# Performance work log

Measured on AMD Instinct MI355X. Metric: run time of the kernel, lower is better.

## Reference

```python
import jax, jax.numpy as jnp
import numpy as np

NEG_SLOPE = 0.2  # PyG GATConv default negative_slope
EPS = 1e-16      # PyG softmax denominator eps


def gat_layer(x, src, dst, W, b, a_src, a_dst, n_nodes):
    # x: [N, Fin]; W: [Fout, Fin]; a_src/a_dst: [Fout] (heads=1, concat)
    h = x @ W.T                                   # [N, Fout]
    al_s = h @ a_src                              # [N]
    al_d = h @ a_dst                              # [N]
    e = jax.nn.leaky_relu(al_s[src] + al_d[dst], NEG_SLOPE)   # [E]
    m = jax.lax.stop_gradient(
        jax.ops.segment_max(e, dst, num_segments=n_nodes))   # stable softmax per target
    ex = jnp.exp(e - m[dst])
    denom = jax.ops.segment_sum(ex, dst, num_segments=n_nodes)
    alpha = ex / (denom[dst] + EPS)               # [E]
    out = jax.ops.segment_sum(alpha[:, None] * h[src], dst, num_segments=n_nodes)
    return out + b


def reference(x, edge_index, W0, b0, asrc0, adst0, W1, b1, asrc1, adst1):
    B, N, _ = x.shape
    # GATConv adds self-loops by default
    loops = jnp.arange(N, dtype=edge_index.dtype)
    src = jnp.concatenate([edge_index[0], loops])
    dst = jnp.concatenate([edge_index[1], loops])

    def per_graph(xb):
        h = jax.nn.relu(gat_layer(xb, src, dst, W0, b0, asrc0, adst0, N))
        h = jax.nn.relu(gat_layer(h, src, dst, W1, b1, asrc1, adst1, N))
        return h

    return jax.vmap(per_graph)(x)  # [B, N, Fout]


def setup_inputs() -> dict:
    key = jax.random.key(0)
    ks = jax.random.split(key, 10)
    B, N, E = 4, 10000, 320000
    F0, F1, F2 = 256, 256, 128
    x = jax.random.normal(ks[0], (B, N, F0), dtype=jnp.float32)
    edge_index = jax.random.randint(ks[1], (2, E), 0, N, dtype=jnp.int64)
    s0 = 1.0 / np.sqrt(F0)
    s1 = 1.0 / np.sqrt(F1)
    return {
        "x": x,
        "edge_index": edge_index,
        "W0": jax.random.normal(ks[2], (F1, F0), dtype=jnp.float32) * s0,
        "b0": jnp.zeros((F1,), dtype=jnp.float32),
        "asrc0": jax.random.normal(ks[3], (F1,), dtype=jnp.float32) * s1,
        "adst0": jax.random.normal(ks[4], (F1,), dtype=jnp.float32) * s1,
        "W1": jax.random.normal(ks[5], (F2, F1), dtype=jnp.float32) * s1,
        "b1": jnp.zeros((F2,), dtype=jnp.float32),
        "asrc1": jax.random.normal(ks[6], (F2,), dtype=jnp.float32) / np.sqrt(F2),
        "adst1": jax.random.normal(ks[7], (F2,), dtype=jnp.float32) / np.sqrt(F2),
    }
```

## Files before the change

### kernel.cpp

```cpp
#include <hip/hip_runtime.h>
#include <hip/hip_bf16.h>

#define NN 10000
#define EE 320000
#define BB 4
#define F0 256
#define F1 256
#define F2 128
#define ETOT (EE + NN)

typedef __attribute__((ext_vector_type(8))) short bf16x8;
typedef __attribute__((ext_vector_type(4))) float f32x4;

__device__ inline unsigned short f2bf_rn(float f) {
    unsigned int u = __float_as_uint(f);
    unsigned int r = (u + 0x7fffu + ((u >> 16) & 1u)) >> 16;
    return (unsigned short)r;
}
__device__ inline float bf2f(unsigned short s) {
    return __uint_as_float(((unsigned int)s) << 16);
}

__global__ void count_kernel(const int* __restrict__ ei, int* __restrict__ deg) {
    int id = blockIdx.x * blockDim.x + threadIdx.x;
    if (id >= ETOT) return;
    int dst = (id < EE) ? ei[EE + id] : (id - EE);
    atomicAdd(&deg[dst], 1);
}

__global__ void scan_kernel(const int* __restrict__ deg, int* __restrict__ rowstart) {
    __shared__ int part[256];
    int t = threadIdx.x;
    const int CH = (NN + 255) / 256;
    int lo = t * CH, hi = min(lo + CH, NN);
    int s = 0;
    for (int i = lo; i < hi; i++) s += deg[i];
    part[t] = s;
    __syncthreads();
    for (int off = 1; off < 256; off <<= 1) {
        int v = (t >= off) ? part[t - off] : 0;
        __syncthreads();
        part[t] += v;
        __syncthreads();
    }
    int run = (t == 0) ? 0 : part[t - 1];
    for (int i = lo; i < hi; i++) { int d = deg[i]; rowstart[i] = run; run += d; }
    if (t == 255) rowstart[NN] = run;
}

__global__ void scatter_kernel(const int* __restrict__ ei,
                               const int* __restrict__ rowstart,
                               int* __restrict__ fill,
                               int* __restrict__ sorted_src) {
    int id = blockIdx.x * blockDim.x + threadIdx.x;
    if (id >= ETOT) return;
    int src, dst;
    if (id < EE) { src = ei[id]; dst = ei[EE + id]; }
    else         { src = dst = id - EE; }
    int pos = rowstart[dst] + atomicAdd(&fill[dst], 1);
    sorted_src[pos] = src;
}

__global__ __launch_bounds__(256) void conv_split(const float* __restrict__ in,
                                                  unsigned short* __restrict__ out2,
                                                  int rows, int K) {
    int q = K >> 2;
    int id = blockIdx.x * blockDim.x + threadIdx.x;
    if (id >= rows * q) return;
    int r = id / q;
    int c4 = (id - r * q) << 2;
    float4 v = *(const float4*)(in + (size_t)r * K + c4);
    ushort4 hi, lo;
    hi.x = f2bf_rn(v.x); lo.x = f2bf_rn(v.x - bf2f(hi.x));
    hi.y = f2bf_rn(v.y); lo.y = f2bf_rn(v.y - bf2f(hi.y));
    hi.z = f2bf_rn(v.z); lo.z = f2bf_rn(v.z - bf2f(hi.z));
    hi.w = f2bf_rn(v.w); lo.w = f2bf_rn(v.w - bf2f(hi.w));
    unsigned short* o = out2 + (size_t)r * 2 * K;
    *(ushort4*)(o + c4) = hi;
    *(ushort4*)(o + K + c4) = lo;
}

__global__ __launch_bounds__(256) void gemm_mfma(const unsigned short* __restrict__ A2,
                                                 const unsigned short* __restrict__ B2,
                                                 unsigned short* __restrict__ C,
                                                 int M, int N, int K) {
    __shared__ short As[128 * 40];
    __shared__ short Bs[128 * 40];
    int tid = threadIdx.x;
    int wave = tid >> 6, lane = tid & 63;
    int wm = wave & 1, wn = wave >> 1;
    int bm = blockIdx.x * 128, bn = blockIdx.y * 128;
    int lq = lane >> 4, lm = lane & 15;
    const int K2 = 2 * K;

    f32x4 acc[4][4];
#pragma unroll
    for (int i = 0; i < 4; i++)
#pragma unroll
        for (int j = 0; j < 4; j++) {
            acc[i][j][0] = 0.f; acc[i][j][1] = 0.f;
            acc[i][j][2] = 0.f; acc[i][j][3] = 0.f;
        }

    int sr = tid >> 2;
    int sc = (tid & 3) << 3;

    for (int t = 0; t < 3; t++) {
        int aoff = (t == 1) ? K : 0;
        int boff = (t == 2) ? K : 0;
        for (int k0 = 0; k0 < K; k0 += 32) {
#pragma unroll
            for (int hh = 0; hh < 2; hh++) {
                int r = sr + hh * 64;
                uint4 va = make_uint4(0, 0, 0, 0);
                int grow = bm + r;
                if (grow < M)
                    va = *(const uint4*)(A2 + (size_t)grow * K2 + aoff + k0 + sc);
                *(uint4*)(As + r * 40 + sc) = va;
                uint4 vb = *(const uint4*)(B2 + (size_t)(bn + r) * K2 + boff + k0 + sc);
                *(uint4*)(Bs + r * 40 + sc) = vb;
            }
            __syncthreads();
            bf16x8 af[4], bfr[4];
#pragma unroll
            for (int i = 0; i < 4; i++) {
                af[i]  = *(const bf16x8*)(As + (wm * 64 + i * 16 + lm) * 40 + lq * 8);
                bfr[i] = *(const bf16x8*)(Bs + (wn * 64 + i * 16 + lm) * 40 + lq * 8);
            }
#pragma unroll
            for (int i = 0; i < 4; i++)
#pragma unroll
                for (int j = 0; j < 4; j++)
                    acc[i][j] = __builtin_amdgcn_mfma_f32_16x16x32_bf16(af[i], bfr[j], acc[i][j], 0, 0, 0);
            __syncthreads();
        }
    }
#pragma unroll
    for (int i = 0; i < 4; i++) {
        int rbase = bm + wm * 64 + i * 16 + lq * 4;
#pragma unroll
        for (int rr = 0; rr < 4; rr++) {
            int row = rbase + rr;
            if (row < M) {
#pragma unroll
                for (int j = 0; j < 4; j++)
                    C[(size_t)row * N + bn + wn * 64 + j * 16 + lm] = f2bf_rn(acc[i][j][rr]);
            }
        }
    }
}

template <int F>
__global__ __launch_bounds__(256) void al_kernel(const unsigned short* __restrict__ h,
                                                 const float* __restrict__ asrc,
                                                 const float* __restrict__ adst,
                                                 float* __restrict__ als,
                                                 float* __restrict__ ald) {
    constexpr int V = F / 64;
    typedef unsigned short usv __attribute__((ext_vector_type(V)));
    int wid = (blockIdx.x * blockDim.x + threadIdx.x) >> 6;
    int lane = threadIdx.x & 63;
    usv hv = *(const usv*)(h + (size_t)wid * F + lane * V);
    float s = 0.f, d = 0.f;
#pragma unroll
    for (int u = 0; u < V; u++) {
        float v = bf2f(hv[u]);
        s += v * asrc[lane * V + u];
        d += v * adst[lane * V + u];
    }
#pragma unroll
    for (int off = 32; off; off >>= 1) {
        s += __shfl_xor(s, off);
        d += __shfl_xor(d, off);
    }
    if (lane == 0) { als[wid] = s; ald[wid] = d; }
}

template <int F, int OUTMODE>
__global__ __launch_bounds__(256) void agg_kernel(const unsigned short* __restrict__ h,
                                                  const float* __restrict__ als,
                                                  const float* __restrict__ ald,
                                                  const int* __restrict__ rowstart,
                                                  const int* __restrict__ sorted_src,
                                                  const float* __restrict__ bias,
                                                  float* __restrict__ out,
                                                  unsigned short* __restrict__ out2) {
    constexpr int V = F / 64;
    typedef unsigned short usv __attribute__((ext_vector_type(V)));
    typedef float fvec __attribute__((ext_vector_type(V)));

    int wid = (blockIdx.x * blockDim.x + threadIdx.x) >> 6;
    int lane = threadIdx.x & 63;
    int b = wid / NN;
    int n = wid - b * NN;

    const float* als_b = als + (size_t)b * NN;
    float aldn = ald[(size_t)b * NN + n];
    int rs = rowstart[n];
    int deg = rowstart[n + 1] - rs;
    const unsigned short* hb = h + (size_t)b * NN * F;

    fvec acc;
#pragma unroll
    for (int u = 0; u < V; u++) acc[u] = 0.f;
    float sum = 0.f;

    for (int c0 = 0; c0 < deg; c0 += 64) {
        int j = c0 + lane;
        float ex = 0.f;
        int srcj = 0;
        if (j < deg) {
            srcj = sorted_src[rs + j];
            float e = als_b[srcj] + aldn;
            e = e > 0.f ? e : 0.2f * e;
            ex = __expf(e);
        }
        sum += ex;
        int cnt = min(64, deg - c0);

        int nfull = cnt >> 4;
        for (int g = 0; g < nfull; g++) {
            int bse = g << 4;
            int s[16]; float w[16];
#pragma unroll
            for (int i = 0; i < 16; i++) {
                s[i] = __shfl(srcj, bse + i);
                w[i] = __shfl(ex, bse + i);
            }
            usv r[16];
#pragma unroll
            for (int i = 0; i < 16; i++)
                r[i] = *(const usv*)(hb + (size_t)s[i] * F + lane * V);
#pragma unroll
            for (int i = 0; i < 16; i++)
#pragma unroll
                for (int u = 0; u < V; u++) acc[u] += w[i] * bf2f(r[i][u]);
        }
        for (int bse = nfull << 4; bse < cnt; bse += 4) {
            int s[4]; float w[4];
#pragma unroll
            for (int i = 0; i < 4; i++) {
                s[i] = __shfl(srcj, bse + i);
                w[i] = __shfl(ex, bse + i);
            }
            usv r[4];
#pragma unroll
            for (int i = 0; i < 4; i++)
                r[i] = *(const usv*)(hb + (size_t)s[i] * F + lane * V);
#pragma unroll
            for (int i = 0; i < 4; i++)
#pragma unroll
                for (int u = 0; u < V; u++) acc[u] += w[i] * bf2f(r[i][u]);
        }
    }
#pragma unroll
    for (int off = 32; off; off >>= 1) sum += __shfl_xor(sum, off);
    float inv = 1.0f / (sum + 1e-16f);

    fvec r;
#pragma unroll
    for (int u = 0; u < V; u++) {
        float v = acc[u] * inv + bias[lane * V + u];
        r[u] = fmaxf(v, 0.f);
    }
    if (OUTMODE == 0) {
        *(fvec*)(out + (size_t)wid * F + lane * V) = r;
    } else {
        ushort4 hi, lo;
        hi.x = f2bf_rn(r[0]); lo.x = f2bf_rn(r[0] - bf2f(hi.x));
        hi.y = f2bf_rn(r[1]); lo.y = f2bf_rn(r[1] - bf2f(hi.y));
        hi.z = f2bf_rn(r[2]); lo.z = f2bf_rn(r[2] - bf2f(hi.z));
        hi.w = f2bf_rn(r[3]); lo.w = f2bf_rn(r[3] - bf2f(hi.w));
        unsigned short* o = out2 + (size_t)wid * 2 * F;
        *(ushort4*)(o + lane * 4) = hi;
        *(ushort4*)(o + F + lane * 4) = lo;
    }
}

extern "C" void kernel_launch(void* const* d_in, const int* in_sizes, int n_in,
                              void* d_out, int out_size, void* d_ws, size_t ws_size,
                              hipStream_t stream) {
    const float* x     = (const float*)d_in[0];
    const int*   ei    = (const int*)d_in[1];
    const float* W0    = (const float*)d_in[2];
    const float* b0    = (const float*)d_in[3];
    const float* asrc0 = (const float*)d_in[4];
    const float* adst0 = (const float*)d_in[5];
    const float* W1    = (const float*)d_in[6];
    const float* b1    = (const float*)d_in[7];
    const float* asrc1 = (const float*)d_in[8];
    const float* adst1 = (const float*)d_in[9];
    float* outp = (float*)d_out;

    const int M = BB * NN;

    size_t off = 0;
    char* base = (char*)d_ws;
    auto alloc = [&](size_t bytes) {
        void* p = base + off;
        off += (bytes + 255) & ~(size_t)255;
        return p;
    };
    int*   deg        = (int*)alloc((size_t)NN * 4);
    int*   fill       = (int*)alloc((size_t)NN * 4);
    int*   rowstart   = (int*)alloc((size_t)(NN + 1) * 4);
    int*   sorted_src = (int*)alloc((size_t)ETOT * 4);
    unsigned short* A2  = (unsigned short*)alloc((size_t)M * 512 * 2);
    unsigned short* W02 = (unsigned short*)alloc((size_t)F1 * 512 * 2);
    unsigned short* W12 = (unsigned short*)alloc((size_t)F2 * 512 * 2);
    unsigned short* h   = (unsigned short*)alloc((size_t)M * F1 * 2);
    float* als        = (float*)alloc((size_t)M * 4);
    float* ald        = (float*)alloc((size_t)M * 4);

    hipMemsetAsync(deg, 0, (size_t)NN * 4, stream);
    hipMemsetAsync(fill, 0, (size_t)NN * 4, stream);

    int egrid = (ETOT + 255) / 256;
    count_kernel<<<egrid, 256, 0, stream>>>(ei, deg);
    scan_kernel<<<1, 256, 0, stream>>>(deg, rowstart);
    scatter_kernel<<<egrid, 256, 0, stream>>>(ei, rowstart, fill, sorted_src);

    int mtiles = (M + 127) / 128;
    int wgrid = (M * 64) / 256;

    conv_split<<<(M * (F0 / 4) + 255) / 256, 256, 0, stream>>>(x, A2, M, F0);
    conv_split<<<(F1 * (F0 / 4) + 255) / 256, 256, 0, stream>>>(W0, W02, F1, F0);
    conv_split<<<(F2 * (F1 / 4) + 255) / 256, 256, 0, stream>>>(W1, W12, F2, F1);

    gemm_mfma<<<dim3(mtiles, F1 / 128), 256, 0, stream>>>(A2, W02, h, M, F1, F0);
    al_kernel<F1><<<wgrid, 256, 0, stream>>>(h, asrc0, adst0, als, ald);
    agg_kernel<F1, 1><<<wgrid, 256, 0, stream>>>(h, als, ald, rowstart, sorted_src, b0,
                                                 nullptr, A2 );

    gemm_mfma<<<dim3(mtiles, F2 / 128), 256, 0, stream>>>(A2, W12, h, M, F2, F1);
    al_kernel<F2><<<wgrid, 256, 0, stream>>>(h, asrc1, adst1, als, ald);
    agg_kernel<F2, 0><<<wgrid, 256, 0, stream>>>(h, als, ald, rowstart, sorted_src, b1,
                                                 outp, nullptr);
}
```

Before: 344.0 us.

## Load GEMM tiles directly into LDS and stage epilogue stores through LDS

```diff
diff --git a/kernel.cpp b/kernel.cpp
--- a/kernel.cpp
+++ b/kernel.cpp
@@ -19,6 +19,12 @@
 }
 __device__ inline float bf2f(unsigned short s) {
     return __uint_as_float(((unsigned int)s) << 16);
+}
+
+__device__ __forceinline__ void gload16(const void* g, void* lds) {
+    __builtin_amdgcn_global_load_lds(
+        (const __attribute__((address_space(1))) unsigned int*)g,
+        (__attribute__((address_space(3))) unsigned int*)lds, 16, 0, 0);
 }
 
 __global__ void count_kernel(const int* __restrict__ ei, int* __restrict__ deg) {
@@ -83,9 +89,11 @@
 __global__ __launch_bounds__(256) void gemm_mfma(const unsigned short* __restrict__ A2,
                                                  const unsigned short* __restrict__ B2,
                                                  unsigned short* __restrict__ C,
+                                                 const unsigned short* __restrict__ zp,
                                                  int M, int N, int K) {
-    __shared__ short As[128 * 40];
-    __shared__ short Bs[128 * 40];
+    __shared__ unsigned short sbuf[8704];
+    unsigned short* As = sbuf;
+    unsigned short* Bs = sbuf + 4096;
     int tid = threadIdx.x;
     int wave = tid >> 6, lane = tid & 63;
     int wm = wave & 1, wn = wave >> 1;
@@ -102,30 +110,31 @@
             acc[i][j][2] = 0.f; acc[i][j][3] = 0.f;
         }
 
-    int sr = tid >> 2;
-    int sc = (tid & 3) << 3;
+    int r0 = tid >> 2;
+    int csh = (tid & 3) << 3;
+    const unsigned short* aP0 = ((bm + r0) < M ? A2 + (size_t)(bm + r0) * K2 : zp) + csh;
+    const unsigned short* aP1 = ((bm + r0 + 64) < M ? A2 + (size_t)(bm + r0 + 64) * K2 : zp) + csh;
+    const unsigned short* bP0 = B2 + (size_t)(bn + r0) * K2 + csh;
+    const unsigned short* bP1 = B2 + (size_t)(bn + r0 + 64) * K2 + csh;
+    unsigned short* ldsA0 = As + tid * 8;
+    unsigned short* ldsA1 = As + (256 + tid) * 8;
+    unsigned short* ldsB0 = Bs + tid * 8;
+    unsigned short* ldsB1 = Bs + (256 + tid) * 8;
 
     for (int t = 0; t < 3; t++) {
         int aoff = (t == 1) ? K : 0;
         int boff = (t == 2) ? K : 0;
         for (int k0 = 0; k0 < K; k0 += 32) {
-#pragma unroll
-            for (int hh = 0; hh < 2; hh++) {
-                int r = sr + hh * 64;
-                uint4 va = make_uint4(0, 0, 0, 0);
-                int grow = bm + r;
-                if (grow < M)
-                    va = *(const uint4*)(A2 + (size_t)grow * K2 + aoff + k0 + sc);
-                *(uint4*)(As + r * 40 + sc) = va;
-                uint4 vb = *(const uint4*)(B2 + (size_t)(bn + r) * K2 + boff + k0 + sc);
-                *(uint4*)(Bs + r * 40 + sc) = vb;
-            }
+            gload16(aP0 + aoff + k0, ldsA0);
+            gload16(aP1 + aoff + k0, ldsA1);
+            gload16(bP0 + boff + k0, ldsB0);
+            gload16(bP1 + boff + k0, ldsB1);
             __syncthreads();
             bf16x8 af[4], bfr[4];
 #pragma unroll
             for (int i = 0; i < 4; i++) {
-                af[i]  = *(const bf16x8*)(As + (wm * 64 + i * 16 + lm) * 40 + lq * 8);
-                bfr[i] = *(const bf16x8*)(Bs + (wn * 64 + i * 16 + lm) * 40 + lq * 8);
+                af[i]  = *(const bf16x8*)(As + (wm * 64 + i * 16 + lm) * 32 + lq * 8);
+                bfr[i] = *(const bf16x8*)(Bs + (wn * 64 + i * 16 + lm) * 32 + lq * 8);
             }
 #pragma unroll
             for (int i = 0; i < 4; i++)
@@ -135,16 +144,31 @@
             __syncthreads();
         }
     }
-#pragma unroll
-    for (int i = 0; i < 4; i++) {
-        int rbase = bm + wm * 64 + i * 16 + lq * 4;
-#pragma unroll
-        for (int rr = 0; rr < 4; rr++) {
-            int row = rbase + rr;
-            if (row < M) {
-#pragma unroll
-                for (int j = 0; j < 4; j++)
-                    C[(size_t)row * N + bn + wn * 64 + j * 16 + lm] = f2bf_rn(acc[i][j][rr]);
+
+    unsigned short* Cs = sbuf;
+    for (int h = 0; h < 2; h++) {
+        __syncthreads();
+        if (wm == h) {
+#pragma unroll
+            for (int i = 0; i < 4; i++) {
+                int rbase = i * 16 + lq * 4;
+#pragma unroll
+                for (int rr = 0; rr < 4; rr++) {
+#pragma unroll
+                    for (int j = 0; j < 4; j++)
+                        Cs[(rbase + rr) * 136 + wn * 64 + j * 16 + lm] = f2bf_rn(acc[i][j][rr]);
+                }
+            }
+        }
+        __syncthreads();
+#pragma unroll
+        for (int r = 0; r < 4; r++) {
+            int u = r * 256 + tid;
+            int row_l = u >> 4, q = u & 15;
+            int row_g = bm + h * 64 + row_l;
+            if (row_g < M) {
+                uint4 v = *(const uint4*)(Cs + row_l * 136 + q * 8);
+                *(uint4*)(C + (size_t)row_g * N + bn + q * 8) = v;
             }
         }
     }
@@ -311,9 +335,11 @@
     unsigned short* h   = (unsigned short*)alloc((size_t)M * F1 * 2);
     float* als        = (float*)alloc((size_t)M * 4);
     float* ald        = (float*)alloc((size_t)M * 4);
+    unsigned short* zp = (unsigned short*)alloc(2048);
 
     hipMemsetAsync(deg, 0, (size_t)NN * 4, stream);
     hipMemsetAsync(fill, 0, (size_t)NN * 4, stream);
+    hipMemsetAsync(zp, 0, 2048, stream);
 
     int egrid = (ETOT + 255) / 256;
     count_kernel<<<egrid, 256, 0, stream>>>(ei, deg);
@@ -327,12 +353,12 @@
     conv_split<<<(F1 * (F0 / 4) + 255) / 256, 256, 0, stream>>>(W0, W02, F1, F0);
     conv_split<<<(F2 * (F1 / 4) + 255) / 256, 256, 0, stream>>>(W1, W12, F2, F1);
 
-    gemm_mfma<<<dim3(mtiles, F1 / 128), 256, 0, stream>>>(A2, W02, h, M, F1, F0);
+    gemm_mfma<<<dim3(mtiles, F1 / 128), 256, 0, stream>>>(A2, W02, h, zp, M, F1, F0);
     al_kernel<F1><<<wgrid, 256, 0, stream>>>(h, asrc0, adst0, als, ald);
     agg_kernel<F1, 1><<<wgrid, 256, 0, stream>>>(h, als, ald, rowstart, sorted_src, b0,
                                                  nullptr, A2 );
 
-    gemm_mfma<<<dim3(mtiles, F2 / 128), 256, 0, stream>>>(A2, W12, h, M, F2, F1);
+    gemm_mfma<<<dim3(mtiles, F2 / 128), 256, 0, stream>>>(A2, W12, h, zp, M, F2, F1);
     al_kernel<F2><<<wgrid, 256, 0, stream>>>(h, asrc1, adst1, als, ald);
     agg_kernel<F2, 0><<<wgrid, 256, 0, stream>>>(h, als, ald, rowstart, sorted_src, b1,
                                                  outp, nullptr);
```

Result: no change. 340.7 us (-1.0%).

## Replace tiled GEMM with skinny 32-row GEMM fused with attention logits

Applied to the files above, without the earlier changes.

```diff
diff --git a/kernel.cpp b/kernel.cpp
--- a/kernel.cpp
+++ b/kernel.cpp
@@ -19,6 +19,12 @@
 }
 __device__ inline float bf2f(unsigned short s) {
     return __uint_as_float(((unsigned int)s) << 16);
+}
+
+__device__ __forceinline__ void gload16(const void* g, void* lds) {
+    __builtin_amdgcn_global_load_lds(
+        (const __attribute__((address_space(1))) unsigned int*)g,
+        (__attribute__((address_space(3))) unsigned int*)lds, 16, 0, 0);
 }
 
 __global__ void count_kernel(const int* __restrict__ ei, int* __restrict__ deg) {
@@ -80,100 +86,108 @@
     *(ushort4*)(o + K + c4) = lo;
 }
 
-__global__ __launch_bounds__(256) void gemm_mfma(const unsigned short* __restrict__ A2,
-                                                 const unsigned short* __restrict__ B2,
-                                                 unsigned short* __restrict__ C,
-                                                 int M, int N, int K) {
-    __shared__ short As[128 * 40];
-    __shared__ short Bs[128 * 40];
+template <int NC>
+__global__ __launch_bounds__(256) void gemm_skinny(
+    const unsigned short* __restrict__ A2,
+    const unsigned short* __restrict__ B2,
+    unsigned short* __restrict__ C,
+    const float* __restrict__ asrc,
+    const float* __restrict__ adst,
+    float* __restrict__ als,
+    float* __restrict__ ald) {
+    constexpr int JT = NC / 64;
+    __shared__ unsigned short sbuf[32 * NC];
+    unsigned short* As = sbuf;
     int tid = threadIdx.x;
     int wave = tid >> 6, lane = tid & 63;
-    int wm = wave & 1, wn = wave >> 1;
-    int bm = blockIdx.x * 128, bn = blockIdx.y * 128;
     int lq = lane >> 4, lm = lane & 15;
-    const int K2 = 2 * K;
-
-    f32x4 acc[4][4];
-#pragma unroll
-    for (int i = 0; i < 4; i++)
-#pragma unroll
-        for (int j = 0; j < 4; j++) {
+    int bm = blockIdx.x * 32;
+
+    f32x4 acc[2][JT];
+#pragma unroll
+    for (int i = 0; i < 2; i++)
+#pragma unroll
+        for (int j = 0; j < JT; j++) {
             acc[i][j][0] = 0.f; acc[i][j][1] = 0.f;
             acc[i][j][2] = 0.f; acc[i][j][3] = 0.f;
         }
 
-    int sr = tid >> 2;
-    int sc = (tid & 3) << 3;
-
-    for (int t = 0; t < 3; t++) {
-        int aoff = (t == 1) ? K : 0;
-        int boff = (t == 2) ? K : 0;
-        for (int k0 = 0; k0 < K; k0 += 32) {
-#pragma unroll
-            for (int hh = 0; hh < 2; hh++) {
-                int r = sr + hh * 64;
-                uint4 va = make_uint4(0, 0, 0, 0);
-                int grow = bm + r;
-                if (grow < M)
-                    va = *(const uint4*)(A2 + (size_t)grow * K2 + aoff + k0 + sc);
-                *(uint4*)(As + r * 40 + sc) = va;
-                uint4 vb = *(const uint4*)(B2 + (size_t)(bn + r) * K2 + boff + k0 + sc);
-                *(uint4*)(Bs + r * 40 + sc) = vb;
+    const unsigned short* aPtr = A2 + (size_t)(bm + (tid >> 3)) * 512 + ((tid & 7) << 3);
+    unsigned short* ldsDst = As + tid * 8;
+
+    const unsigned short* bRow[JT];
+#pragma unroll
+    for (int j = 0; j < JT; j++)
+        bRow[j] = B2 + (size_t)(wave * (NC / 4) + j * 16 + lm) * 512 + lq * 8;
+
+#pragma unroll
+    for (int ph = 0; ph < 2; ph++) {
+        int aoff = ph * 256;
+#pragma unroll
+        for (int k0 = 0; k0 < 256; k0 += 64) {
+            gload16(aPtr + aoff + k0, ldsDst);
+            __syncthreads();
+#pragma unroll
+            for (int kk = 0; kk < 2; kk++) {
+                bf16x8 af0 = *(const bf16x8*)(As + lm * 64 + kk * 32 + lq * 8);
+                bf16x8 af1 = *(const bf16x8*)(As + (16 + lm) * 64 + kk * 32 + lq * 8);
+#pragma unroll
+                for (int j = 0; j < JT; j++) {
+                    bf16x8 bh = *(const bf16x8*)(bRow[j] + k0 + kk * 32);
+                    acc[0][j] = __builtin_amdgcn_mfma_f32_16x16x32_bf16(af0, bh, acc[0][j], 0, 0, 0);
+                    acc[1][j] = __builtin_amdgcn_mfma_f32_16x16x32_bf16(af1, bh, acc[1][j], 0, 0, 0);
+                }
+                if (ph == 0) {
+#pragma unroll
+                    for (int j = 0; j < JT; j++) {
+                        bf16x8 bl = *(const bf16x8*)(bRow[j] + 256 + k0 + kk * 32);
+                        acc[0][j] = __builtin_amdgcn_mfma_f32_16x16x32_bf16(af0, bl, acc[0][j], 0, 0, 0);
+                        acc[1][j] = __builtin_amdgcn_mfma_f32_16x16x32_bf16(af1, bl, acc[1][j], 0, 0, 0);
+                    }
+                }
             }
             __syncthreads();
-            bf16x8 af[4], bfr[4];
-#pragma unroll
-            for (int i = 0; i < 4; i++) {
-                af[i]  = *(const bf16x8*)(As + (wm * 64 + i * 16 + lm) * 40 + lq * 8);
-                bfr[i] = *(const bf16x8*)(Bs + (wn * 64 + i * 16 + lm) * 40 + lq * 8);
+        }
+    }
+
+    unsigned short* Cs = sbuf;
+#pragma unroll
+    for (int i = 0; i < 2; i++)
+#pragma unroll
+        for (int rr = 0; rr < 4; rr++) {
+            int row = i * 16 + lq * 4 + rr;
+#pragma unroll
+            for (int j = 0; j < JT; j++)
+                Cs[row * NC + wave * (NC / 4) + j * 16 + lm] = f2bf_rn(acc[i][j][rr]);
+        }
+    __syncthreads();
+
+    {
+        int r = tid >> 3;
+        int cseg = (tid & 7) * (NC / 8);
+        float s = 0.f, d = 0.f;
+#pragma unroll
+        for (int c8 = 0; c8 < NC / 64; c8++) {
+            bf16x8 v8 = *(const bf16x8*)(Cs + r * NC + cseg + c8 * 8);
+#pragma unroll
+            for (int u = 0; u < 8; u++) {
+                float v = bf2f((unsigned short)v8[u]);
+                s += v * asrc[cseg + c8 * 8 + u];
+                d += v * adst[cseg + c8 * 8 + u];
             }
-#pragma unroll
-            for (int i = 0; i < 4; i++)
-#pragma unroll
-                for (int j = 0; j < 4; j++)
-                    acc[i][j] = __builtin_amdgcn_mfma_f32_16x16x32_bf16(af[i], bfr[j], acc[i][j], 0, 0, 0);
-            __syncthreads();
-        }
-    }
-#pragma unroll
-    for (int i = 0; i < 4; i++) {
-        int rbase = bm + wm * 64 + i * 16 + lq * 4;
-#pragma unroll
-        for (int rr = 0; rr < 4; rr++) {
-            int row = rbase + rr;
-            if (row < M) {
-#pragma unroll
-                for (int j = 0; j < 4; j++)
-                    C[(size_t)row * N + bn + wn * 64 + j * 16 + lm] = f2bf_rn(acc[i][j][rr]);
-            }
-        }
-    }
-}
-
-template <int F>
-__global__ __launch_bounds__(256) void al_kernel(const unsigned short* __restrict__ h,
-                                                 const float* __restrict__ asrc,
-                                                 const float* __restrict__ adst,
-                                                 float* __restrict__ als,
-                                                 float* __restrict__ ald) {
-    constexpr int V = F / 64;
-    typedef unsigned short usv __attribute__((ext_vector_type(V)));
-    int wid = (blockIdx.x * blockDim.x + threadIdx.x) >> 6;
-    int lane = threadIdx.x & 63;
-    usv hv = *(const usv*)(h + (size_t)wid * F + lane * V);
-    float s = 0.f, d = 0.f;
-#pragma unroll
-    for (int u = 0; u < V; u++) {
-        float v = bf2f(hv[u]);
-        s += v * asrc[lane * V + u];
-        d += v * adst[lane * V + u];
-    }
-#pragma unroll
-    for (int off = 32; off; off >>= 1) {
-        s += __shfl_xor(s, off);
-        d += __shfl_xor(d, off);
-    }
-    if (lane == 0) { als[wid] = s; ald[wid] = d; }
+        }
+        s += __shfl_xor(s, 1); d += __shfl_xor(d, 1);
+        s += __shfl_xor(s, 2); d += __shfl_xor(d, 2);
+        s += __shfl_xor(s, 4); d += __shfl_xor(d, 4);
+        if ((tid & 7) == 0) { als[bm + r] = s; ald[bm + r] = d; }
+    }
+
+#pragma unroll
+    for (int u0 = 0; u0 < NC / 64; u0++) {
+        int u = u0 * 256 + tid;
+        int row = u / (NC / 8), q = u % (NC / 8);
+        *(uint4*)(C + (size_t)(bm + row) * NC + q * 8) = *(const uint4*)(Cs + row * NC + q * 8);
+    }
 }
 
 template <int F, int OUTMODE>
@@ -189,13 +203,16 @@
     typedef unsigned short usv __attribute__((ext_vector_type(V)));
     typedef float fvec __attribute__((ext_vector_type(V)));
 
-    int wid = (blockIdx.x * blockDim.x + threadIdx.x) >> 6;
+    int bx = blockIdx.x;
+    int xcd = bx & 7;
+    int b = xcd >> 1;
+    int ng = ((bx >> 3) << 1) | (xcd & 1);
+    int n = ng * 4 + (threadIdx.x >> 6);
     int lane = threadIdx.x & 63;
-    int b = wid / NN;
-    int n = wid - b * NN;
+    int wid = b * NN + n;
 
     const float* als_b = als + (size_t)b * NN;
-    float aldn = ald[(size_t)b * NN + n];
+    float aldn = ald[wid];
     int rs = rowstart[n];
     int deg = rowstart[n + 1] - rs;
     const unsigned short* hb = h + (size_t)b * NN * F;
@@ -312,28 +329,24 @@
     float* als        = (float*)alloc((size_t)M * 4);
     float* ald        = (float*)alloc((size_t)M * 4);
 
-    hipMemsetAsync(deg, 0, (size_t)NN * 4, stream);
-    hipMemsetAsync(fill, 0, (size_t)NN * 4, stream);
+    hipMemsetAsync(deg, 0, (char*)fill - (char*)deg + (size_t)NN * 4, stream);
 
     int egrid = (ETOT + 255) / 256;
     count_kernel<<<egrid, 256, 0, stream>>>(ei, deg);
     scan_kernel<<<1, 256, 0, stream>>>(deg, rowstart);
     scatter_kernel<<<egrid, 256, 0, stream>>>(ei, rowstart, fill, sorted_src);
 
-    int mtiles = (M + 127) / 128;
     int wgrid = (M * 64) / 256;
 
     conv_split<<<(M * (F0 / 4) + 255) / 256, 256, 0, stream>>>(x, A2, M, F0);
     conv_split<<<(F1 * (F0 / 4) + 255) / 256, 256, 0, stream>>>(W0, W02, F1, F0);
     conv_split<<<(F2 * (F1 / 4) + 255) / 256, 256, 0, stream>>>(W1, W12, F2, F1);
 
-    gemm_mfma<<<dim3(mtiles, F1 / 128), 256, 0, stream>>>(A2, W02, h, M, F1, F0);
-    al_kernel<F1><<<wgrid, 256, 0, stream>>>(h, asrc0, adst0, als, ald);
+    gemm_skinny<F1><<<M / 32, 256, 0, stream>>>(A2, W02, h, asrc0, adst0, als, ald);
     agg_kernel<F1, 1><<<wgrid, 256, 0, stream>>>(h, als, ald, rowstart, sorted_src, b0,
                                                  nullptr, A2 );
 
-    gemm_mfma<<<dim3(mtiles, F2 / 128), 256, 0, stream>>>(A2, W12, h, M, F2, F1);
-    al_kernel<F2><<<wgrid, 256, 0, stream>>>(h, asrc1, adst1, als, ald);
+    gemm_skinny<F2><<<M / 32, 256, 0, stream>>>(A2, W12, h, asrc1, adst1, als, ald);
     agg_kernel<F2, 0><<<wgrid, 256, 0, stream>>>(h, als, ald, rowstart, sorted_src, b1,
                                                  outp, nullptr);
 }
```

Measured after the change: 370.9 us. +7.8%, slower.

## Fuse attention logits into register-prefetched split-bf16 GEMM with staged epilogue

Applied to the files above, without the earlier changes.

```diff
diff --git a/kernel.cpp b/kernel.cpp
--- a/kernel.cpp
+++ b/kernel.cpp
@@ -80,18 +80,28 @@
     *(ushort4*)(o + K + c4) = lo;
 }
 
-__global__ __launch_bounds__(256) void gemm_mfma(const unsigned short* __restrict__ A2,
-                                                 const unsigned short* __restrict__ B2,
-                                                 unsigned short* __restrict__ C,
-                                                 int M, int N, int K) {
-    __shared__ short As[128 * 40];
-    __shared__ short Bs[128 * 40];
+template <int NT>
+__global__ __launch_bounds__(256) void gemm_db(
+    const unsigned short* __restrict__ A2,
+    const unsigned short* __restrict__ B2,
+    unsigned short* __restrict__ C,
+    const float* __restrict__ asrc,
+    const float* __restrict__ adst,
+    float* __restrict__ als,
+    float* __restrict__ ald,
+    int M) {
+    __shared__ unsigned short sbuf[20480];
+    unsigned short* Ah = sbuf;
+    unsigned short* Al = sbuf + 5120;
+    unsigned short* Bh = sbuf + 10240;
+    unsigned short* Bl = sbuf + 15360;
+
     int tid = threadIdx.x;
     int wave = tid >> 6, lane = tid & 63;
     int wm = wave & 1, wn = wave >> 1;
-    int bm = blockIdx.x * 128, bn = blockIdx.y * 128;
     int lq = lane >> 4, lm = lane & 15;
-    const int K2 = 2 * K;
+    int bm = blockIdx.x * 128;
+    int bn = blockIdx.y * 128;
 
     f32x4 acc[4][4];
 #pragma unroll
@@ -102,78 +112,103 @@
             acc[i][j][2] = 0.f; acc[i][j][3] = 0.f;
         }
 
-    int sr = tid >> 2;
-    int sc = (tid & 3) << 3;
-
-    for (int t = 0; t < 3; t++) {
-        int aoff = (t == 1) ? K : 0;
-        int boff = (t == 2) ? K : 0;
-        for (int k0 = 0; k0 < K; k0 += 32) {
-#pragma unroll
-            for (int hh = 0; hh < 2; hh++) {
-                int r = sr + hh * 64;
-                uint4 va = make_uint4(0, 0, 0, 0);
-                int grow = bm + r;
-                if (grow < M)
-                    va = *(const uint4*)(A2 + (size_t)grow * K2 + aoff + k0 + sc);
-                *(uint4*)(As + r * 40 + sc) = va;
-                uint4 vb = *(const uint4*)(B2 + (size_t)(bn + r) * K2 + boff + k0 + sc);
-                *(uint4*)(Bs + r * 40 + sc) = vb;
+    int r0 = tid >> 2, sub = tid & 3;
+    int ar0 = min(bm + r0, M - 1), ar1 = min(bm + r0 + 64, M - 1);
+    const unsigned short* aSrc0 = A2 + (size_t)ar0 * 512 + sub * 8;
+    const unsigned short* aSrc1 = A2 + (size_t)ar1 * 512 + sub * 8;
+    const unsigned short* bSrc0 = B2 + (size_t)(bn + r0) * 512 + sub * 8;
+    const unsigned short* bSrc1 = B2 + (size_t)(bn + r0 + 64) * 512 + sub * 8;
+    int ld0 = r0 * 40 + sub * 8;
+    int ld1 = (r0 + 64) * 40 + sub * 8;
+
+    uint4 pAh0, pAh1, pAl0, pAl1, pBh0, pBh1, pBl0, pBl1;
+
+    auto loadreg = [&](int c) {
+        int o = c * 32;
+        pAh0 = *(const uint4*)(aSrc0 + o);       pAh1 = *(const uint4*)(aSrc1 + o);
+        pAl0 = *(const uint4*)(aSrc0 + 256 + o); pAl1 = *(const uint4*)(aSrc1 + 256 + o);
+        pBh0 = *(const uint4*)(bSrc0 + o);       pBh1 = *(const uint4*)(bSrc1 + o);
+        pBl0 = *(const uint4*)(bSrc0 + 256 + o); pBl1 = *(const uint4*)(bSrc1 + 256 + o);
+    };
+    auto writereg = [&]() {
+        *(uint4*)(Ah + ld0) = pAh0; *(uint4*)(Ah + ld1) = pAh1;
+        *(uint4*)(Al + ld0) = pAl0; *(uint4*)(Al + ld1) = pAl1;
+        *(uint4*)(Bh + ld0) = pBh0; *(uint4*)(Bh + ld1) = pBh1;
+        *(uint4*)(Bl + ld0) = pBl0; *(uint4*)(Bl + ld1) = pBl1;
+    };
+
+    loadreg(0);
+#pragma unroll 1
+    for (int c = 0; c < 8; c++) {
+        __syncthreads();
+        writereg();
+        __syncthreads();
+        if (c < 7) loadreg(c + 1);
+
+        bf16x8 afh[4], afl[4];
+#pragma unroll
+        for (int i = 0; i < 4; i++) {
+            int row = wm * 64 + i * 16 + lm;
+            afh[i] = *(const bf16x8*)(Ah + row * 40 + lq * 8);
+            afl[i] = *(const bf16x8*)(Al + row * 40 + lq * 8);
+        }
+#pragma unroll
+        for (int j = 0; j < 4; j++) {
+            int row = wn * 64 + j * 16 + lm;
+            bf16x8 bh = *(const bf16x8*)(Bh + row * 40 + lq * 8);
+            bf16x8 bl = *(const bf16x8*)(Bl + row * 40 + lq * 8);
+#pragma unroll
+            for (int i = 0; i < 4; i++) {
+                acc[i][j] = __builtin_amdgcn_mfma_f32_16x16x32_bf16(afh[i], bh, acc[i][j], 0, 0, 0);
+                acc[i][j] = __builtin_amdgcn_mfma_f32_16x16x32_bf16(afl[i], bh, acc[i][j], 0, 0, 0);
+                acc[i][j] = __builtin_amdgcn_mfma_f32_16x16x32_bf16(afh[i], bl, acc[i][j], 0, 0, 0);
             }
-            __syncthreads();
-            bf16x8 af[4], bfr[4];
-#pragma unroll
-            for (int i = 0; i < 4; i++) {
-                af[i]  = *(const bf16x8*)(As + (wm * 64 + i * 16 + lm) * 40 + lq * 8);
-                bfr[i] = *(const bf16x8*)(Bs + (wn * 64 + i * 16 + lm) * 40 + lq * 8);
+        }
+    }
+
+    __syncthreads();
+
+    unsigned short* Cs = sbuf;
+#pragma unroll
+    for (int i = 0; i < 4; i++) {
+#pragma unroll
+        for (int rr = 0; rr < 4; rr++) {
+            int row = wm * 64 + i * 16 + lq * 4 + rr;
+#pragma unroll
+            for (int j = 0; j < 4; j++)
+                Cs[row * 136 + wn * 64 + j * 16 + lm] = f2bf_rn(acc[i][j][rr]);
+        }
+    }
+    __syncthreads();
+
+    {
+        int r = tid >> 1;
+        int cl = (tid & 1) * 64;
+        float s = 0.f, d = 0.f;
+#pragma unroll
+        for (int c8 = 0; c8 < 8; c8++) {
+            bf16x8 v8 = *(const bf16x8*)(Cs + r * 136 + cl + c8 * 8);
+#pragma unroll
+            for (int u = 0; u < 8; u++) {
+                float v = bf2f((unsigned short)v8[u]);
+                s += v * asrc[bn + cl + c8 * 8 + u];
+                d += v * adst[bn + cl + c8 * 8 + u];
             }
-#pragma unroll
-            for (int i = 0; i < 4; i++)
-#pragma unroll
-                for (int j = 0; j < 4; j++)
-                    acc[i][j] = __builtin_amdgcn_mfma_f32_16x16x32_bf16(af[i], bfr[j], acc[i][j], 0, 0, 0);
-            __syncthreads();
-        }
-    }
-#pragma unroll
-    for (int i = 0; i < 4; i++) {
-        int rbase = bm + wm * 64 + i * 16 + lq * 4;
-#pragma unroll
-        for (int rr = 0; rr < 4; rr++) {
-            int row = rbase + rr;
-            if (row < M) {
-#pragma unroll
-                for (int j = 0; j < 4; j++)
-                    C[(size_t)row * N + bn + wn * 64 + j * 16 + lm] = f2bf_rn(acc[i][j][rr]);
-            }
-        }
-    }
-}
-
-template <int F>
-__global__ __launch_bounds__(256) void al_kernel(const unsigned short* __restrict__ h,
-                                                 const float* __restrict__ asrc,
-                                                 const float* __restrict__ adst,
-                                                 float* __restrict__ als,
-                                                 float* __restrict__ ald) {
-    constexpr int V = F / 64;
-    typedef unsigned short usv __attribute__((ext_vector_type(V)));
-    int wid = (blockIdx.x * blockDim.x + threadIdx.x) >> 6;
-    int lane = threadIdx.x & 63;
-    usv hv = *(const usv*)(h + (size_t)wid * F + lane * V);
-    float s = 0.f, d = 0.f;
-#pragma unroll
-    for (int u = 0; u < V; u++) {
-        float v = bf2f(hv[u]);
-        s += v * asrc[lane * V + u];
-        d += v * adst[lane * V + u];
-    }
-#pragma unroll
-    for (int off = 32; off; off >>= 1) {
-        s += __shfl_xor(s, off);
-        d += __shfl_xor(d, off);
-    }
-    if (lane == 0) { als[wid] = s; ald[wid] = d; }
+        }
+        s += __shfl_xor(s, 1); d += __shfl_xor(d, 1);
+        if ((tid & 1) == 0 && (bm + r) < M) {
+            atomicAdd(&als[bm + r], s);
+            atomicAdd(&ald[bm + r], d);
+        }
+    }
+
+#pragma unroll
+    for (int k = 0; k < 8; k++) {
+        int u = k * 256 + tid;
+        int row = u >> 4, q = u & 15;
+        if (bm + row < M)
+            *(uint4*)(C + (size_t)(bm + row) * NT + bn + q * 8) = *(const uint4*)(Cs + row * 136 + q * 8);
+    }
 }
 
 template <int F, int OUTMODE>
@@ -195,7 +230,7 @@
     int n = wid - b * NN;
 
     const float* als_b = als + (size_t)b * NN;
-    float aldn = ald[(size_t)b * NN + n];
+    float aldn = ald[wid];
     int rs = rowstart[n];
     int deg = rowstart[n + 1] - rs;
     const unsigned short* hb = h + (size_t)b * NN * F;
@@ -312,28 +347,28 @@
     float* als        = (float*)alloc((size_t)M * 4);
     float* ald        = (float*)alloc((size_t)M * 4);
 
-    hipMemsetAsync(deg, 0, (size_t)NN * 4, stream);
-    hipMemsetAsync(fill, 0, (size_t)NN * 4, stream);
+    hipMemsetAsync(deg, 0, (char*)fill - (char*)deg + (size_t)NN * 4, stream);
 
     int egrid = (ETOT + 255) / 256;
     count_kernel<<<egrid, 256, 0, stream>>>(ei, deg);
     scan_kernel<<<1, 256, 0, stream>>>(deg, rowstart);
     scatter_kernel<<<egrid, 256, 0, stream>>>(ei, rowstart, fill, sorted_src);
 
-    int mtiles = (M + 127) / 128;
     int wgrid = (M * 64) / 256;
 
     conv_split<<<(M * (F0 / 4) + 255) / 256, 256, 0, stream>>>(x, A2, M, F0);
     conv_split<<<(F1 * (F0 / 4) + 255) / 256, 256, 0, stream>>>(W0, W02, F1, F0);
     conv_split<<<(F2 * (F1 / 4) + 255) / 256, 256, 0, stream>>>(W1, W12, F2, F1);
 
-    gemm_mfma<<<dim3(mtiles, F1 / 128), 256, 0, stream>>>(A2, W02, h, M, F1, F0);
-    al_kernel<F1><<<wgrid, 256, 0, stream>>>(h, asrc0, adst0, als, ald);
+    int mtiles = (M + 127) / 128;
+
+    hipMemsetAsync(als, 0, (size_t)2 * M * 4, stream);
+    gemm_db<F1><<<dim3(mtiles, F1 / 128), 256, 0, stream>>>(A2, W02, h, asrc0, adst0, als, ald, M);
     agg_kernel<F1, 1><<<wgrid, 256, 0, stream>>>(h, als, ald, rowstart, sorted_src, b0,
                                                  nullptr, A2 );
 
-    gemm_mfma<<<dim3(mtiles, F2 / 128), 256, 0, stream>>>(A2, W12, h, M, F2, F1);
-    al_kernel<F2><<<wgrid, 256, 0, stream>>>(h, asrc1, adst1, als, ald);
+    hipMemsetAsync(als, 0, (size_t)2 * M * 4, stream);
+    gemm_db<F2><<<dim3(mtiles, F2 / 128), 256, 0, stream>>>(A2, W12, h, asrc1, adst1, als, ald, M);
     agg_kernel<F2, 0><<<wgrid, 256, 0, stream>>>(h, als, ald, rowstart, sorted_src, b1,
                                                  outp, nullptr);
 }
```

New measurement: 322.9 us. 6.1% less time.
